# Optimization experiments

Hardware: AMD Instinct MI355X
Metric: run time of the kernel (lower is better)

Reference implementation:

```python
import jax, jax.numpy as jnp
import numpy as np

COMMITMENT_COST = 0.25


def setup_inputs() -> dict:
    key = jax.random.key(0)
    k1, k2 = jax.random.split(key)
    B, C, H, W, D = 8, 64, 32, 32, 32
    NUM_EMB = 512
    x = jax.random.normal(k1, (B, C, H, W, D), dtype=jnp.float32)
    # torch init: uniform(-1/num_embeddings, 1/num_embeddings)
    codebook = jax.random.uniform(k2, (NUM_EMB, C), dtype=jnp.float32,
                                  minval=-1.0 / NUM_EMB, maxval=1.0 / NUM_EMB)
    return {"x": x, "codebook": codebook}


def reference(x, codebook):
    B, C, H, W, D = x.shape
    # [B,C,H,W,D] -> [N, C] with N = B*H*W*D
    flat = jnp.transpose(x, (0, 2, 3, 4, 1)).reshape(-1, C)
    # squared L2 distances to every codebook entry: [N, num_embeddings]
    dist = (jnp.sum(flat * flat, axis=1, keepdims=True)
            - 2.0 * flat @ codebook.T
            + jnp.sum(codebook * codebook, axis=1))
    idx = jnp.argmin(dist, axis=1)                     # [N]
    # one-hot @ codebook  ==  gather (same math, efficient form)
    quant_flat = codebook[idx]                          # [N, C]
    quant = jnp.transpose(quant_flat.reshape(B, H, W, D, C), (0, 4, 1, 2, 3))
    e_loss = jnp.mean((jax.lax.stop_gradient(quant) - x) ** 2)
    q_loss = jnp.mean((quant - jax.lax.stop_gradient(x)) ** 2)
    loss = q_loss + COMMITMENT_COST * e_loss
    # straight-through estimator
    quant_st = x + jax.lax.stop_gradient(quant - x)
    return quant_st, loss
```

## Files before the change

kernel.cpp:

```cpp
#include <hip/hip_runtime.h>
#include <cstdint>
#include <cstddef>

#define SPATIAL   32768
#define CHANNELS  64
#define NUM_EMB   512
#define NPOS      262144
#define OUT_ELEMS 16777216
#define BLOCK     256
#define POSB      128
#define LOSS_SCALE (1.25f / 16777216.0f)

typedef __attribute__((ext_vector_type(8))) short bf16x8;
typedef __attribute__((ext_vector_type(4))) float f32x4;

union b8u { int i[4]; bf16x8 v; };
union fiu { float f; unsigned u; };

__device__ __forceinline__ short f2bf_rne(float f) {
    fiu v; v.f = f;
    unsigned r = v.u + 0x7fffu + ((v.u >> 16) & 1u);
    return (short)(r >> 16);
}

__global__ void vq_prep(const float* __restrict__ cb,
                        short* __restrict__ cbfrag,
                        float* __restrict__ cbn,
                        float* __restrict__ loss_slot) {
    int e = blockIdx.x * blockDim.x + threadIdx.x;
    if (e == 0) *loss_slot = 0.0f;
    if (e < NUM_EMB) {
        const int nt  = e >> 4;
        const int col = e & 15;
        float s = 0.0f;
#pragma unroll
        for (int q = 0; q < 4; ++q) {
#pragma unroll
            for (int j = 0; j < 8; ++j) {
                float v0 = cb[e * CHANNELS + q * 8 + j];
                float v1 = cb[e * CHANNELS + 32 + q * 8 + j];
                cbfrag[nt * 1024 + (q * 16 + col) * 8 + j]       = f2bf_rne(v0);
                cbfrag[nt * 1024 + 512 + (q * 16 + col) * 8 + j] = f2bf_rne(v1);
            }
        }
#pragma unroll
        for (int c = 0; c < CHANNELS; ++c) {
            float v = cb[e * CHANNELS + c];
            s = __builtin_fmaf(v, v, s);
        }
        cbn[e] = -0.5f * s;
    }
}

__global__ __launch_bounds__(BLOCK, 6) void vq_main(
    const float* __restrict__ x,
    const float* __restrict__ cb,
    const short* __restrict__ cbfrag,
    const float* __restrict__ cbn,
    float* __restrict__ out,
    float* __restrict__ loss_slot) {
#pragma clang fp contract(off)
    __shared__ __align__(16) char arena[16384];
    __shared__ int   cand[POSB];
    __shared__ float wsum[4];

    short* stageS = (short*)arena;
    float* qbuf   = (float*)arena;

    const int tid  = threadIdx.x;
    const int wave = tid >> 6, lane = tid & 63;
    const int q    = lane >> 4, col = lane & 15;

    const int blockPos = blockIdx.x * POSB;
    const int b     = blockPos >> 15;
    const int sbase = blockPos & 32767;
    const float* xb = x + (size_t)b * (CHANNELS * SPATIAL);
    const int wbase = sbase + wave * 32;

#pragma unroll
    for (int rd = 0; rd < 2; ++rd) {
        const int off = rd * 4096 + wave * 1024;
        __builtin_amdgcn_global_load_lds(
            (const __attribute__((address_space(1))) unsigned*)
                ((const char*)cbfrag + off + lane * 16),
            (__attribute__((address_space(3))) unsigned*)(arena + off), 16, 0, 0);
    }
    __builtin_amdgcn_sched_barrier(0);

    b8u A[2][2];
#pragma unroll
    for (int t = 0; t < 2; ++t) {
        const unsigned* pu = (const unsigned*)xb + (wbase + t * 16 + col);
#pragma unroll
        for (int kh = 0; kh < 2; ++kh)
#pragma unroll
            for (int jj = 0; jj < 4; ++jj) {
                unsigned u0 = pu[(size_t)(kh * 32 + q * 8 + 2 * jj + 0) * SPATIAL];
                unsigned u1 = pu[(size_t)(kh * 32 + q * 8 + 2 * jj + 1) * SPATIAL];
                A[t][kh].i[jj] = __builtin_amdgcn_perm(u1, u0, 0x07060302u);
            }
    }

    __syncthreads();

    float mt[2];
    mt[0] = -3.4e38f; mt[1] = -3.4e38f;
    const unsigned MASK = 0xFFFFFE00u;

    int buf = 0;
#pragma unroll 1
    for (int c = 0; c < 8; ++c) {
        if (c < 7) {
#pragma unroll
            for (int rd = 0; rd < 2; ++rd) {
                const int off = rd * 4096 + wave * 1024;
                __builtin_amdgcn_global_load_lds(
                    (const __attribute__((address_space(1))) unsigned*)
                        ((const char*)cbfrag + (c + 1) * 8192 + off + lane * 16),
                    (__attribute__((address_space(3))) unsigned*)
                        (arena + (buf ^ 1) * 8192 + off), 16, 0, 0);
            }
        }
#pragma unroll
        for (int k = 0; k < 4; ++k) {
            const int nt = c * 4 + k;
            const short* sb = stageS + buf * 4096 + k * 1024 + (lane << 3);
            bf16x8 CB0 = *(const bf16x8*)sb;
            bf16x8 CB1 = *(const bf16x8*)(sb + 512);
            f32x4 civ  = *(const f32x4*)(cbn + nt * 16 + (q << 2));
            const unsigned encq = (unsigned)(511 - nt * 16 - (q << 2));
#pragma unroll
            for (int tt = 0; tt < 2; ++tt) {
                f32x4 acc = __builtin_amdgcn_mfma_f32_16x16x32_bf16(CB0, A[tt][0].v, civ, 0, 0, 0);
                acc = __builtin_amdgcn_mfma_f32_16x16x32_bf16(CB1, A[tt][1].v, acc, 0, 0, 0);
                fiu p0, p1, p2, p3;
                p0.f = acc[0]; p0.u = (p0.u & MASK) | (encq - 0);
                p1.f = acc[1]; p1.u = (p1.u & MASK) | (encq - 1);
                p2.f = acc[2]; p2.u = (p2.u & MASK) | (encq - 2);
                p3.f = acc[3]; p3.u = (p3.u & MASK) | (encq - 3);
                float mm = fmaxf(fmaxf(p0.f, p1.f), fmaxf(p2.f, p3.f));
                mt[tt] = fmaxf(mt[tt], mm);
            }
        }
        __syncthreads();
        buf ^= 1;
    }

#pragma unroll
    for (int t = 0; t < 2; ++t) {
        float v = mt[t];
        v = fmaxf(v, __shfl_xor(v, 16, 64));
        v = fmaxf(v, __shfl_xor(v, 32, 64));
        if (lane < 16) {
            fiu p; p.f = v;
            cand[wave * 32 + t * 16 + lane] = 511 - (int)(p.u & 511u);
        }
    }
    __syncthreads();

    const int pos = tid & (POSB - 1);
    const int sub = tid >> 7;
    const int gr  = tid >> 3;
    const int gl  = tid & 7;
    const float* pxb = xb + (sbase + pos);
    float* opb = out + (size_t)b * (CHANNELS * SPATIAL) + (sbase + pos);
    float lsum = 0.0f;

#pragma unroll 1
    for (int cc = 0; cc < 2; ++cc) {
#pragma unroll
        for (int rd = 0; rd < 4; ++rd) {
            const int r   = rd * 32 + gr;
            const int row = cand[r];
            f32x4 v = *((const f32x4*)(cb + (size_t)row * CHANNELS + cc * 32) + gl);
            *((f32x4*)(qbuf + r * 32 + ((gl ^ (r & 7)) << 2))) = v;
        }
        __syncthreads();
#pragma unroll
        for (int j = 0; j < 4; ++j) {
            const int jj = sub * 4 + j;
            f32x4 qq = *((const f32x4*)(qbuf + pos * 32 + ((jj ^ (pos & 7)) << 2)));
#pragma unroll
            for (int k = 0; k < 4; ++k) {
                const int ch = cc * 32 + jj * 4 + k;
                float xv = pxb[(size_t)ch * SPATIAL];
                float t2 = qq[k] - xv;
                opb[(size_t)ch * SPATIAL] = xv + t2;
                lsum = __builtin_fmaf(t2, t2, lsum);
            }
        }
        if (cc == 0) __syncthreads();
    }

#pragma unroll
    for (int off = 32; off > 0; off >>= 1) lsum += __shfl_down(lsum, off, 64);
    if (lane == 0) wsum[wave] = lsum;
    __syncthreads();
    if (tid == 0) {
        float bs = (wsum[0] + wsum[1]) + (wsum[2] + wsum[3]);
        atomicAdd(loss_slot, bs * LOSS_SCALE);
    }
}

extern "C" void kernel_launch(void* const* d_in, const int* in_sizes, int n_in,
                              void* d_out, int out_size, void* d_ws, size_t ws_size,
                              hipStream_t stream) {
    const float* x  = (const float*)d_in[0];
    const float* cb = (const float*)d_in[1];
    float* out = (float*)d_out;
    short* cbfrag = (short*)d_ws;
    float* cbn    = (float*)(cbfrag + NUM_EMB * CHANNELS);
    float* loss_slot = out + OUT_ELEMS;

    vq_prep<<<2, 256, 0, stream>>>(cb, cbfrag, cbn, loss_slot);
    vq_main<<<NPOS / POSB, BLOCK, 0, stream>>>(x, cb, cbfrag, cbn, out, loss_slot);
}
```

Before: 153.3 us.

## Double positions per block and reuse register-held x for the output pass

Each block now handles 256 positions instead of 128, with each wave computing four 16-position MFMA tiles per codebook chunk. This halves codebook staging traffic per position. The raw fp32 x values loaded for the bf16 A fragments stay in registers and are reused in the epilogue, so x is no longer re-read from global memory. Codebook norms are staged into LDS, and max3 instructions shorten the argmax reduction. The costs are higher register pressure (launch bounds drop to 4 blocks), a larger LDS footprint and half as many blocks.

```diff
diff --git a/kernel.cpp b/kernel.cpp
--- a/kernel.cpp
+++ b/kernel.cpp
@@ -8,7 +8,7 @@
 #define NPOS      262144
 #define OUT_ELEMS 16777216
 #define BLOCK     256
-#define POSB      128
+#define POSB      256
 #define LOSS_SCALE (1.25f / 16777216.0f)
 
 typedef __attribute__((ext_vector_type(8))) short bf16x8;
@@ -16,6 +16,12 @@
 
 union b8u { int i[4]; bf16x8 v; };
 union fiu { float f; unsigned u; };
+
+__device__ __forceinline__ float max3f(float a, float b, float c) {
+    float d;
+    asm("v_max3_f32 %0, %1, %2, %3" : "=v"(d) : "v"(a), "v"(b), "v"(c));
+    return d;
+}
 
 __device__ __forceinline__ short f2bf_rne(float f) {
     fiu v; v.f = f;
@@ -52,7 +58,7 @@
     }
 }
 
-__global__ __launch_bounds__(BLOCK, 6) void vq_main(
+__global__ __launch_bounds__(BLOCK, 4) void vq_main(
     const float* __restrict__ x,
     const float* __restrict__ cb,
     const short* __restrict__ cbfrag,
@@ -60,7 +66,8 @@
     float* __restrict__ out,
     float* __restrict__ loss_slot) {
 #pragma clang fp contract(off)
-    __shared__ __align__(16) char arena[16384];
+    __shared__ __align__(16) char arena[32768];
+    __shared__ float cbnL[NUM_EMB];
     __shared__ int   cand[POSB];
     __shared__ float wsum[4];
 
@@ -75,36 +82,53 @@
     const int b     = blockPos >> 15;
     const int sbase = blockPos & 32767;
     const float* xb = x + (size_t)b * (CHANNELS * SPATIAL);
-    const int wbase = sbase + wave * 32;
+    const int wbase = sbase + wave * 64;
 
 #pragma unroll
     for (int rd = 0; rd < 2; ++rd) {
-        const int off = rd * 4096 + wave * 1024;
         __builtin_amdgcn_global_load_lds(
             (const __attribute__((address_space(1))) unsigned*)
-                ((const char*)cbfrag + off + lane * 16),
-            (__attribute__((address_space(3))) unsigned*)(arena + off), 16, 0, 0);
+                ((const char*)cbfrag + rd * 4096 + tid * 16),
+            (__attribute__((address_space(3))) unsigned*)
+                (arena + rd * 4096 + tid * 16), 16, 0, 0);
+    }
+#pragma unroll
+    for (int rd = 0; rd < 2; ++rd) {
+        __builtin_amdgcn_global_load_lds(
+            (const __attribute__((address_space(1))) unsigned*)(cbn + rd * 256 + tid),
+            (__attribute__((address_space(3))) unsigned*)(cbnL + rd * 256 + tid),
+            4, 0, 0);
     }
     __builtin_amdgcn_sched_barrier(0);
 
-    b8u A[2][2];
-#pragma unroll
-    for (int t = 0; t < 2; ++t) {
+    unsigned xr[4][2][4][2];
+#pragma unroll
+    for (int t = 0; t < 4; ++t) {
         const unsigned* pu = (const unsigned*)xb + (wbase + t * 16 + col);
 #pragma unroll
         for (int kh = 0; kh < 2; ++kh)
 #pragma unroll
             for (int jj = 0; jj < 4; ++jj) {
-                unsigned u0 = pu[(size_t)(kh * 32 + q * 8 + 2 * jj + 0) * SPATIAL];
-                unsigned u1 = pu[(size_t)(kh * 32 + q * 8 + 2 * jj + 1) * SPATIAL];
-                A[t][kh].i[jj] = __builtin_amdgcn_perm(u1, u0, 0x07060302u);
-            }
-    }
+                xr[t][kh][jj][0] = pu[(size_t)(kh * 32 + q * 8 + 2 * jj + 0) * SPATIAL];
+                xr[t][kh][jj][1] = pu[(size_t)(kh * 32 + q * 8 + 2 * jj + 1) * SPATIAL];
+            }
+    }
+
+    b8u A[4][2];
+#pragma unroll
+    for (int t = 0; t < 4; ++t)
+#pragma unroll
+        for (int kh = 0; kh < 2; ++kh)
+#pragma unroll
+            for (int jj = 0; jj < 4; ++jj)
+                A[t][kh].i[jj] = __builtin_amdgcn_perm(
+                    xr[t][kh][jj][1], xr[t][kh][jj][0], 0x07060302u);
 
     __syncthreads();
 
-    float mt[2];
-    mt[0] = -3.4e38f; mt[1] = -3.4e38f;
+    float mt[4];
+#pragma unroll
+    for (int t = 0; t < 4; ++t) mt[t] = -3.4e38f;
     const unsigned MASK = 0xFFFFFE00u;
 
     int buf = 0;
@@ -113,12 +137,11 @@
         if (c < 7) {
 #pragma unroll
             for (int rd = 0; rd < 2; ++rd) {
-                const int off = rd * 4096 + wave * 1024;
                 __builtin_amdgcn_global_load_lds(
                     (const __attribute__((address_space(1))) unsigned*)
-                        ((const char*)cbfrag + (c + 1) * 8192 + off + lane * 16),
+                        ((const char*)cbfrag + (c + 1) * 8192 + rd * 4096 + tid * 16),
                     (__attribute__((address_space(3))) unsigned*)
-                        (arena + (buf ^ 1) * 8192 + off), 16, 0, 0);
+                        (arena + (buf ^ 1) * 8192 + rd * 4096 + tid * 16), 16, 0, 0);
             }
         }
 #pragma unroll
@@ -127,10 +150,10 @@
             const short* sb = stageS + buf * 4096 + k * 1024 + (lane << 3);
             bf16x8 CB0 = *(const bf16x8*)sb;
             bf16x8 CB1 = *(const bf16x8*)(sb + 512);
-            f32x4 civ  = *(const f32x4*)(cbn + nt * 16 + (q << 2));
+            f32x4 civ  = *(const f32x4*)(cbnL + nt * 16 + (q << 2));
             const unsigned encq = (unsigned)(511 - nt * 16 - (q << 2));
 #pragma unroll
-            for (int tt = 0; tt < 2; ++tt) {
+            for (int tt = 0; tt < 4; ++tt) {
                 f32x4 acc = __builtin_amdgcn_mfma_f32_16x16x32_bf16(CB0, A[tt][0].v, civ, 0, 0, 0);
                 acc = __builtin_amdgcn_mfma_f32_16x16x32_bf16(CB1, A[tt][1].v, acc, 0, 0, 0);
                 fiu p0, p1, p2, p3;
@@ -138,8 +161,8 @@
                 p1.f = acc[1]; p1.u = (p1.u & MASK) | (encq - 1);
                 p2.f = acc[2]; p2.u = (p2.u & MASK) | (encq - 2);
                 p3.f = acc[3]; p3.u = (p3.u & MASK) | (encq - 3);
-                float mm = fmaxf(fmaxf(p0.f, p1.f), fmaxf(p2.f, p3.f));
-                mt[tt] = fmaxf(mt[tt], mm);
+                float pm = max3f(p0.f, p1.f, p2.f);
+                mt[tt] = max3f(pm, p3.f, mt[tt]);
             }
         }
         __syncthreads();
@@ -147,29 +170,26 @@
     }
 
 #pragma unroll
-    for (int t = 0; t < 2; ++t) {
+    for (int t = 0; t < 4; ++t) {
         float v = mt[t];
         v = fmaxf(v, __shfl_xor(v, 16, 64));
         v = fmaxf(v, __shfl_xor(v, 32, 64));
         if (lane < 16) {
             fiu p; p.f = v;
-            cand[wave * 32 + t * 16 + lane] = 511 - (int)(p.u & 511u);
+            cand[wave * 64 + t * 16 + lane] = 511 - (int)(p.u & 511u);
         }
     }
     __syncthreads();
 
-    const int pos = tid & (POSB - 1);
-    const int sub = tid >> 7;
-    const int gr  = tid >> 3;
-    const int gl  = tid & 7;
-    const float* pxb = xb + (sbase + pos);
-    float* opb = out + (size_t)b * (CHANNELS * SPATIAL) + (sbase + pos);
+    const int gr = tid >> 3;
+    const int gl = tid & 7;
+    float* opb = out + (size_t)b * (CHANNELS * SPATIAL) + (sbase + wave * 64 + col);
     float lsum = 0.0f;
 
-#pragma unroll 1
+#pragma unroll
     for (int cc = 0; cc < 2; ++cc) {
 #pragma unroll
-        for (int rd = 0; rd < 4; ++rd) {
+        for (int rd = 0; rd < 8; ++rd) {
             const int r   = rd * 32 + gr;
             const int row = cand[r];
             f32x4 v = *((const f32x4*)(cb + (size_t)row * CHANNELS + cc * 32) + gl);
@@ -177,16 +197,25 @@
         }
         __syncthreads();
 #pragma unroll
-        for (int j = 0; j < 4; ++j) {
-            const int jj = sub * 4 + j;
-            f32x4 qq = *((const f32x4*)(qbuf + pos * 32 + ((jj ^ (pos & 7)) << 2)));
-#pragma unroll
-            for (int k = 0; k < 4; ++k) {
-                const int ch = cc * 32 + jj * 4 + k;
-                float xv = pxb[(size_t)ch * SPATIAL];
-                float t2 = qq[k] - xv;
-                opb[(size_t)ch * SPATIAL] = xv + t2;
-                lsum = __builtin_fmaf(t2, t2, lsum);
+        for (int t = 0; t < 4; ++t) {
+            const int p  = wave * 64 + t * 16 + col;
+            const int c0 = (2 * q) ^ (p & 7);
+            const int c1 = (2 * q + 1) ^ (p & 7);
+            f32x4 qq0 = *((const f32x4*)(qbuf + p * 32 + (c0 << 2)));
+            f32x4 qq1 = *((const f32x4*)(qbuf + p * 32 + (c1 << 2)));
+            float* opt = opb + t * 16;
+#pragma unroll
+            for (int jj = 0; jj < 4; ++jj) {
+#pragma unroll
+                for (int s = 0; s < 2; ++s) {
+                    const int w  = 2 * jj + s;
+                    const int ch = cc * 32 + q * 8 + w;
+                    float xv = __uint_as_float(xr[t][cc][jj][s]);
+                    float qv = (w < 4) ? qq0[w] : qq1[w - 4];
+                    float t2 = qv - xv;
+                    opt[(size_t)ch * SPATIAL] = xv + t2;
+                    lsum = __builtin_fmaf(t2, t2, lsum);
+                }
             }
         }
         if (cc == 0) __syncthreads();
```

Measured after the change: 137.5 us. 10.3% less time.
